# Kernel tuning notes

Hardware: AMD Instinct MI355X
Metric: run time of the kernel (lower is better)

## Reference

```python
import jax, jax.numpy as jnp
import numpy as np

LN_EPS = 1e-5


def _layernorm(x, w, b):
    mu = jnp.mean(x, axis=-1, keepdims=True)
    var = jnp.mean(jnp.square(x - mu), axis=-1, keepdims=True)
    return (x - mu) * jax.lax.rsqrt(var + LN_EPS) * w + b


def setup_inputs() -> dict:
    key = jax.random.key(0)
    ks = jax.random.split(key, 6)
    B, V, P, D = 32, 4, 784, 768
    H = 8
    x = jax.random.normal(ks[0], (B, V * P, D), dtype=jnp.float32)
    s = 0.02  # init scale for weights
    return {
        "x": x,
        "num_views": V,
        "norm1_w": jnp.ones((D,), jnp.float32),
        "norm1_b": jnp.zeros((D,), jnp.float32),
        "in_proj_w": jax.random.normal(ks[1], (3 * D, D), jnp.float32) * s,
        "in_proj_b": jnp.zeros((3 * D,), jnp.float32),
        "out_w": jax.random.normal(ks[2], (D, D), jnp.float32) * s,
        "out_b": jnp.zeros((D,), jnp.float32),
        "norm2_w": jnp.ones((D,), jnp.float32),
        "norm2_b": jnp.zeros((D,), jnp.float32),
        "ffn_w1": jax.random.normal(ks[3], (4 * D, D), jnp.float32) * s,
        "ffn_b1": jnp.zeros((4 * D,), jnp.float32),
        "ffn_w2": jax.random.normal(ks[4], (D, 4 * D), jnp.float32) * s,
        "ffn_b2": jnp.zeros((D,), jnp.float32),
    }


def reference(x, num_views, norm1_w, norm1_b, in_proj_w, in_proj_b, out_w, out_b,
              norm2_w, norm2_b, ffn_w1, ffn_b1, ffn_w2, ffn_b2):
    B, T, D = x.shape
    V = num_views
    P = T // V
    H = 8
    dh = D // H

    # The per-patch python loop in the original is embarrassingly parallel over
    # patches: fold the patch dim into batch -> (B*P, V, D) tokens of seq-len V.
    xv = x.reshape(B, V, P, D).transpose(0, 2, 1, 3).reshape(B * P, V, D)

    # pre-norm cross-view attention (torch MultiheadAttention, batch_first)
    h = _layernorm(xv, norm1_w, norm1_b)
    qkv = h @ in_proj_w.T + in_proj_b                      # (BP, V, 3D)
    q, k, v = jnp.split(qkv, 3, axis=-1)
    q = q.reshape(B * P, V, H, dh).transpose(0, 2, 1, 3)   # (BP, H, V, dh)
    k = k.reshape(B * P, V, H, dh).transpose(0, 2, 1, 3)
    v = v.reshape(B * P, V, H, dh).transpose(0, 2, 1, 3)
    scores = jnp.einsum("bhqd,bhkd->bhqk", q, k) / jnp.sqrt(jnp.float32(dh))
    attn = jax.nn.softmax(scores, axis=-1)
    o = jnp.einsum("bhqk,bhkd->bhqd", attn, v)             # (BP, H, V, dh)
    o = o.transpose(0, 2, 1, 3).reshape(B * P, V, D)
    o = o @ out_w.T + out_b
    xv = xv + o

    # pre-norm FFN with exact (erf) GELU; dropout = identity (eval mode)
    h = _layernorm(xv, norm2_w, norm2_b)
    h = jax.nn.gelu(h @ ffn_w1.T + ffn_b1, approximate=False)
    xv = xv + (h @ ffn_w2.T + ffn_b2)

    # undo the fold: (BP, V, D) -> (B, P, V, D) -> (B, V, P, D) -> (B, T, D)
    return xv.reshape(B, P, V, D).transpose(0, 2, 1, 3).reshape(B, T, D)
```

## Files before the change

### kernel.cpp

```cpp
#include <hip/hip_runtime.h>
#include <hip/hip_bf16.h>
#include <math.h>

typedef __bf16 bf16x8 __attribute__((ext_vector_type(8)));
typedef float  f32x4  __attribute__((ext_vector_type(4)));
typedef unsigned short us8 __attribute__((ext_vector_type(8)));
typedef unsigned short us4 __attribute__((ext_vector_type(4)));
typedef unsigned short ush;

__device__ __forceinline__ unsigned short f2bf(float x) {
  unsigned int u = __float_as_uint(x);
  u += 0x7FFFu + ((u >> 16) & 1u);
  return (unsigned short)(u >> 16);
}
__device__ __forceinline__ float bf2f(unsigned short v) {
  return __uint_as_float(((unsigned int)v) << 16);
}
__device__ __forceinline__ float gelu_t(float x) {
  float y = 0.7978845608028654f * x * (1.0f + 0.044715f * x * x);
  float e = __expf(2.0f * y);
  return x - x / (e + 1.0f);
}


__global__ __launch_bounds__(256) void conv_f32_bf16(const float* __restrict__ s,
                                                     unsigned short* __restrict__ d, int n4) {
  int i = blockIdx.x * 256 + threadIdx.x;
  if (i >= n4) return;
  float4 f = ((const float4*)s)[i];
  ushort4 u;
  u.x = f2bf(f.x); u.y = f2bf(f.y); u.z = f2bf(f.z); u.w = f2bf(f.w);
  ((ushort4*)d)[i] = u;
}

__global__ __launch_bounds__(256) void ln_kernel(const float* __restrict__ src,
                                                 const float* __restrict__ w,
                                                 const float* __restrict__ b,
                                                 unsigned short* __restrict__ dst) {
  const int wv = threadIdx.x >> 6;
  const int lane = threadIdx.x & 63;
  const int n = blockIdx.x * 4 + wv;
  const int bp = n >> 2, v = n & 3;
  const int bb = bp / 784, p = bp - bb * 784;
  const float* row = src + ((size_t)bb * 3136 + (size_t)v * 784 + p) * 768;
  float4 x0 = ((const float4*)row)[lane];
  float4 x1 = ((const float4*)row)[lane + 64];
  float4 x2 = ((const float4*)row)[lane + 128];
  float s  = x0.x + x0.y + x0.z + x0.w + x1.x + x1.y + x1.z + x1.w
           + x2.x + x2.y + x2.z + x2.w;
  float ss = x0.x*x0.x + x0.y*x0.y + x0.z*x0.z + x0.w*x0.w
           + x1.x*x1.x + x1.y*x1.y + x1.z*x1.z + x1.w*x1.w
           + x2.x*x2.x + x2.y*x2.y + x2.z*x2.z + x2.w*x2.w;
  #pragma unroll
  for (int off = 32; off > 0; off >>= 1) {
    s  += __shfl_xor(s,  off, 64);
    ss += __shfl_xor(ss, off, 64);
  }
  const float mu   = s * (1.0f / 768.0f);
  const float rstd = rsqrtf(ss * (1.0f / 768.0f) - mu * mu + 1e-5f);
  unsigned short* drow = dst + (size_t)n * 768;
  #pragma unroll
  for (int seg = 0; seg < 3; ++seg) {
    float4 xs = (seg == 0) ? x0 : (seg == 1) ? x1 : x2;
    float4 w4 = ((const float4*)w)[lane + seg * 64];
    float4 b4 = ((const float4*)b)[lane + seg * 64];
    ushort4 u;
    u.x = f2bf((xs.x - mu) * rstd * w4.x + b4.x);
    u.y = f2bf((xs.y - mu) * rstd * w4.y + b4.y);
    u.z = f2bf((xs.z - mu) * rstd * w4.z + b4.z);
    u.w = f2bf((xs.w - mu) * rstd * w4.w + b4.w);
    ((ushort4*)drow)[lane + seg * 64] = u;
  }
}


#define BARX() do { asm volatile("" ::: "memory"); \
                    __builtin_amdgcn_s_barrier();  \
                    asm volatile("" ::: "memory"); } while (0)
#define WAITVM(N) asm volatile("s_waitcnt vmcnt(" #N ")" ::: "memory")

#define STAGE(ISB, HALF, TT) do {                                             \
  const ush* _g = (ISB) ? gB : gA;                                            \
  const int _l0 = (((TT) & 1) << 15) + ((ISB) ? 16384 : 0) + ((HALF) << 13)   \
                + (w << 9);                                                   \
  const size_t _go = (size_t)(((HALF) << 7) + (w << 3)) * K                   \
                   + ((size_t)(TT) << 6);                                     \
  __builtin_amdgcn_global_load_lds(                                           \
      (const __attribute__((address_space(1))) void*)(_g + _go),              \
      (__attribute__((address_space(3))) void*)(smem + _l0), 16, 0, 0);       \
  __builtin_amdgcn_global_load_lds(                                           \
      (const __attribute__((address_space(1))) void*)(_g + _go + ((size_t)K << 6)), \
      (__attribute__((address_space(3))) void*)(smem + _l0 + 4096), 16, 0, 0);\
} while (0)

#define LDA(HM) do {                                                          \
  _Pragma("unroll")                                                           \
  for (int mi4 = 0; mi4 < 4; ++mi4) {                                         \
    const int m = wm * 64 + (HM) * 128 + mi4 * 16 + l16;                      \
    _Pragma("unroll")                                                         \
    for (int kk = 0; kk < 2; ++kk) {                                          \
      const int q = kk * 4 + quad;                                            \
      af[mi4][kk] = *(const bf16x8*)(smem + aofs + m * 64 + ((q ^ l7) << 3)); \
    }                                                                         \
  }                                                                           \
} while (0)

#define LDB(HN, BF) do {                                                      \
  _Pragma("unroll")                                                           \
  for (int ni2 = 0; ni2 < 2; ++ni2) {                                         \
    const int n = wn * 32 + (HN) * 128 + ni2 * 16 + l16;                      \
    _Pragma("unroll")                                                         \
    for (int kk = 0; kk < 2; ++kk) {                                          \
      const int q = kk * 4 + quad;                                            \
      BF[ni2][kk] = *(const bf16x8*)(smem + bofs + n * 64 + ((q ^ l7) << 3)); \
    }                                                                         \
  }                                                                           \
} while (0)

#define MFMAC(HM, HN, BF) do {                                                \
  __builtin_amdgcn_s_setprio(1);                                              \
  _Pragma("unroll")                                                           \
  for (int mi4 = 0; mi4 < 4; ++mi4)                                           \
    _Pragma("unroll")                                                         \
    for (int ni2 = 0; ni2 < 2; ++ni2)                                         \
      _Pragma("unroll")                                                       \
      for (int kk = 0; kk < 2; ++kk)                                          \
        acc[(HM)*4 + mi4][(HN)*2 + ni2] = __builtin_amdgcn_mfma_f32_16x16x32_bf16( \
            af[mi4][kk], BF[ni2][kk], acc[(HM)*4 + mi4][(HN)*2 + ni2], 0, 0, 0); \
  __builtin_amdgcn_s_setprio(0);                                              \
} while (0)

template <int K, int EPI>
__global__ __launch_bounds__(512, 2) void gemm256(const ush* __restrict__ A,
                                                  const ush* __restrict__ Bm,
                                                  const float* __restrict__ bias,
                                                  void* __restrict__ outp,
                                                  const float* __restrict__ aux,
                                                  int N) {
  __shared__ __attribute__((aligned(16))) ush smem[65536];
  constexpr int NT = K / 64;
  const int tid  = threadIdx.x;
  const int w    = tid >> 6;
  const int lane = tid & 63;
  const int quad = lane >> 4;
  const int l16  = lane & 15;
  const int l7   = l16 & 7;
  const int wm   = w >> 2;
  const int wn   = w & 3;

  const int gx   = gridDim.x;
  const int nwg  = gx * 392;
  const int flat = blockIdx.y * gx + blockIdx.x;
  const int xcd  = flat & 7;
  const int pos  = xcd * (nwg >> 3) + (flat >> 3);
  const int by   = pos / gx;
  const int bx   = pos - by * gx;

  const int r8  = lane >> 3;
  const int cb  = lane & 7;
  const int swo = (cb ^ r8) << 3;
  const ush* gA = A  + (size_t)(by * 256 + r8) * K + swo;
  const ush* gB = Bm + (size_t)(bx * 256 + r8) * K + swo;

  f32x4 acc[8][4];
  #pragma unroll
  for (int i = 0; i < 8; ++i)
    #pragma unroll
    for (int j = 0; j < 4; ++j) {
      f32x4 z = {0.0f, 0.0f, 0.0f, 0.0f};
      acc[i][j] = z;
    }
  bf16x8 af[4][2], bf0[2][2], bf1[2][2];

  STAGE(0, 0, 0); STAGE(1, 0, 0); STAGE(0, 1, 0);
  STAGE(1, 1, 0); STAGE(0, 0, 1); STAGE(1, 0, 1);
  WAITVM(8);
  BARX();

  #pragma unroll 2
  for (int t = 0; t < NT; ++t) {
    const int aofs = (t & 1) << 15;
    const int bofs = aofs + 16384;
    LDA(0); LDB(0, bf0);
    if (t <= NT - 2) STAGE(0, 1, t + 1);
    BARX();
    MFMAC(0, 0, bf0);
    if (t < NT - 1) { WAITVM(6); } else { WAITVM(0); }
    BARX();
    LDB(1, bf1);
    if (t <= NT - 2) STAGE(1, 1, t + 1);
    BARX();
    MFMAC(0, 1, bf1);
    BARX();
    LDA(1);
    if (t <= NT - 3) STAGE(0, 0, t + 2);
    BARX();
    MFMAC(1, 0, bf0);
    BARX();
    if (t <= NT - 3) STAGE(1, 0, t + 2);
    BARX();
    MFMAC(1, 1, bf1);
    if (t <= NT - 3)      { WAITVM(8); }
    else if (t == NT - 2) { WAITVM(4); }
    BARX();
  }

  float* lsm = (float*)smem;
  #pragma unroll
  for (int s = 0; s < 4; ++s) {
    if (wm == (s & 1)) {
      const int hm = s >> 1;
      #pragma unroll
      for (int mi4 = 0; mi4 < 4; ++mi4)
        #pragma unroll
        for (int ni = 0; ni < 4; ++ni) {
          const int col = wn * 32 + (ni >> 1) * 128 + (ni & 1) * 16 + l16;
          #pragma unroll
          for (int r = 0; r < 4; ++r) {
            const int row_l = mi4 * 16 + quad * 4 + r;
            lsm[row_l * 260 + col] = acc[hm * 4 + mi4][ni][r];
          }
        }
    }
    __syncthreads();
    #pragma unroll
    for (int j = 0; j < 8; ++j) {
      const int cc    = tid + 512 * j;
      const int row_l = cc >> 6;
      const int c4    = (cc & 63) << 2;
      f32x4 vv = *(const f32x4*)&lsm[row_l * 260 + c4];
      const int rr    = by * 256 + s * 64 + row_l;
      const int col_g = bx * 256 + c4;
      f32x4 b4 = *(const f32x4*)&bias[col_g];
      vv += b4;
      if (EPI == 0) {
        const int seg = col_g / 768;
        const int c2  = col_g - seg * 768;
        const int hh  = c2 / 96;
        const int dd  = c2 - hh * 96;
        const int bp = rr >> 2, v = rr & 3;
        us4 u = { f2bf(vv[0]), f2bf(vv[1]), f2bf(vv[2]), f2bf(vv[3]) };
        *(us4*)((unsigned short*)outp + (size_t)bp * 9216 + seg * 3072 + hh * 384 + v * 96 + dd) = u;
      } else if (EPI == 1 || EPI == 3) {
        const int bp = rr >> 2, v = rr & 3;
        const int bb = bp / 784, p = bp - bb * 784;
        const size_t addr = ((size_t)bb * 3136 + (size_t)v * 784 + p) * 768 + col_g;
        f32x4 a4 = *(const f32x4*)(aux + addr);
        vv += a4;
        *(f32x4*)((float*)outp + addr) = vv;
      } else {
        us4 u = { f2bf(gelu_t(vv[0])), f2bf(gelu_t(vv[1])),
                  f2bf(gelu_t(vv[2])), f2bf(gelu_t(vv[3])) };
        *(us4*)((unsigned short*)outp + (size_t)rr * N + col_g) = u;
      }
    }
    __syncthreads();
  }
}

__global__ __launch_bounds__(256) void attn_kernel(const unsigned short* __restrict__ qs,
                                                   unsigned short* __restrict__ o) {
  int idx = blockIdx.x * 256 + threadIdx.x;
  int vq = idx & 3;
  int h  = (idx >> 2) & 7;
  int bp = idx >> 5;
  const unsigned short* qp = qs + (size_t)bp * 9216 + h * 384 + vq * 96;
  const unsigned short* kp = qs + (size_t)bp * 9216 + 3072 + h * 384;
  const unsigned short* vp = qs + (size_t)bp * 9216 + 6144 + h * 384;
  float s0 = 0.f, s1 = 0.f, s2 = 0.f, s3 = 0.f;
  #pragma unroll
  for (int c = 0; c < 96; c += 8) {
    us8 q8 = *(const us8*)(qp + c);
    us8 k0 = *(const us8*)(kp + c);
    us8 k1 = *(const us8*)(kp + 96 + c);
    us8 k2 = *(const us8*)(kp + 192 + c);
    us8 k3 = *(const us8*)(kp + 288 + c);
    #pragma unroll
    for (int j = 0; j < 8; ++j) {
      float qf = bf2f(q8[j]);
      s0 += qf * bf2f(k0[j]);
      s1 += qf * bf2f(k1[j]);
      s2 += qf * bf2f(k2[j]);
      s3 += qf * bf2f(k3[j]);
    }
  }
  const float scale = 0.10206207261596575f;
  s0 *= scale; s1 *= scale; s2 *= scale; s3 *= scale;
  float m = fmaxf(fmaxf(s0, s1), fmaxf(s2, s3));
  float e0 = __expf(s0 - m), e1 = __expf(s1 - m), e2 = __expf(s2 - m), e3 = __expf(s3 - m);
  float inv = 1.0f / (e0 + e1 + e2 + e3);
  e0 *= inv; e1 *= inv; e2 *= inv; e3 *= inv;
  unsigned short* op = o + (size_t)(bp * 4 + vq) * 768 + h * 96;
  #pragma unroll
  for (int c = 0; c < 96; c += 8) {
    us8 v0 = *(const us8*)(vp + c);
    us8 v1 = *(const us8*)(vp + 96 + c);
    us8 v2 = *(const us8*)(vp + 192 + c);
    us8 v3 = *(const us8*)(vp + 288 + c);
    us8 r;
    #pragma unroll
    for (int j = 0; j < 8; ++j) {
      float val = e0 * bf2f(v0[j]) + e1 * bf2f(v1[j]) + e2 * bf2f(v2[j]) + e3 * bf2f(v3[j]);
      r[j] = f2bf(val);
    }
    *(us8*)(op + c) = r;
  }
}

extern "C" void kernel_launch(void* const* d_in, const int* in_sizes, int n_in,
                              void* d_out, int out_size, void* d_ws, size_t ws_size,
                              hipStream_t stream) {
  const float* x         = (const float*)d_in[0];
  const float* norm1_w   = (const float*)d_in[2];
  const float* norm1_b   = (const float*)d_in[3];
  const float* in_proj_w = (const float*)d_in[4];
  const float* in_proj_b = (const float*)d_in[5];
  const float* out_w     = (const float*)d_in[6];
  const float* out_b     = (const float*)d_in[7];
  const float* norm2_w   = (const float*)d_in[8];
  const float* norm2_b   = (const float*)d_in[9];
  const float* ffn_w1    = (const float*)d_in[10];
  const float* ffn_b1    = (const float*)d_in[11];
  const float* ffn_w2    = (const float*)d_in[12];
  const float* ffn_b2    = (const float*)d_in[13];
  float* out = (float*)d_out;

  char* ws = (char*)d_ws;
  unsigned short* wq = (unsigned short*)ws;
  unsigned short* wh = (unsigned short*)(ws + 616562688u);
  unsigned short* wB = (unsigned short*)(ws + 616562688u + 154140672u);
  unsigned short* wIn  = wB;
  unsigned short* wOut = wB + 1769472;
  unsigned short* wF1  = wOut + 589824;
  unsigned short* wF2  = wF1 + 2359296;

  conv_f32_bf16<<<(442368 + 255) / 256, 256, 0, stream>>>(in_proj_w, wIn, 442368);
  conv_f32_bf16<<<(147456 + 255) / 256, 256, 0, stream>>>(out_w, wOut, 147456);
  conv_f32_bf16<<<(589824 + 255) / 256, 256, 0, stream>>>(ffn_w1, wF1, 589824);
  conv_f32_bf16<<<(589824 + 255) / 256, 256, 0, stream>>>(ffn_w2, wF2, 589824);

  ln_kernel<<<25088, 256, 0, stream>>>(x, norm1_w, norm1_b, wh);
  gemm256<768, 0><<<dim3(9, 392), 512, 0, stream>>>(wh, wIn, in_proj_b, (void*)wq, nullptr, 2304);
  attn_kernel<<<3136, 256, 0, stream>>>(wq, wh);
  gemm256<768, 1><<<dim3(3, 392), 512, 0, stream>>>(wh, wOut, out_b, (void*)out, x, 768);
  ln_kernel<<<25088, 256, 0, stream>>>(out, norm2_w, norm2_b, wh);
  gemm256<768, 2><<<dim3(12, 392), 512, 0, stream>>>(wh, wF1, ffn_b1, (void*)wq, nullptr, 3072);
  gemm256<3072, 3><<<dim3(3, 392), 512, 0, stream>>>(wq, wF2, ffn_b2, (void*)out, out, 768);

  (void)in_sizes; (void)n_in; (void)out_size; (void)ws_size;
}
```

Baseline: 2.644 ms.

## Make GEMMs persistent with cross-tile prefetch and direct-register epilogue

Replaces the one-block-per-tile GEMM launch with a persistent kernel of 256 blocks. Each block walks a contiguous range of tiles within its XCD and prefetches the next tile's K-slices while finishing the current one, hiding per-tile prologue and tail latency. The epilogue now writes accumulators straight from registers with scalar stores instead of staging them through LDS, which removes barriers but loses vectorized, coalesced stores. The pointer-advance and wait-count logic becomes more complex, and load balance depends on tile counts per XCD.

```diff
diff --git a/kernel.cpp b/kernel.cpp
--- a/kernel.cpp
+++ b/kernel.cpp
@@ -79,17 +79,15 @@
                     asm volatile("" ::: "memory"); } while (0)
 #define WAITVM(N) asm volatile("s_waitcnt vmcnt(" #N ")" ::: "memory")
 
-#define STAGE(ISB, HALF, TT) do {                                             \
-  const ush* _g = (ISB) ? gB : gA;                                            \
-  const int _l0 = (((TT) & 1) << 15) + ((ISB) ? 16384 : 0) + ((HALF) << 13)   \
+#define STAGE2(ISB, HALF, PAR, PTR) do {                                      \
+  const int _l0 = ((PAR) << 15) + ((ISB) ? 16384 : 0) + ((HALF) << 13)        \
                 + (w << 9);                                                   \
-  const size_t _go = (size_t)(((HALF) << 7) + (w << 3)) * K                   \
-                   + ((size_t)(TT) << 6);                                     \
+  const ush* _g = (PTR) + (size_t)(((HALF) << 7) + (w << 3)) * K;             \
   __builtin_amdgcn_global_load_lds(                                           \
-      (const __attribute__((address_space(1))) void*)(_g + _go),              \
+      (const __attribute__((address_space(1))) void*)_g,                      \
       (__attribute__((address_space(3))) void*)(smem + _l0), 16, 0, 0);       \
   __builtin_amdgcn_global_load_lds(                                           \
-      (const __attribute__((address_space(1))) void*)(_g + _go + ((size_t)K << 6)), \
+      (const __attribute__((address_space(1))) void*)(_g + ((size_t)K << 6)), \
       (__attribute__((address_space(3))) void*)(smem + _l0 + 4096), 16, 0, 0);\
 } while (0)
 
@@ -130,13 +128,146 @@
   __builtin_amdgcn_s_setprio(0);                                              \
 } while (0)
 
+#define ZEROACC() do {                                                        \
+  _Pragma("unroll")                                                           \
+  for (int _i = 0; _i < 8; ++_i)                                              \
+    _Pragma("unroll")                                                         \
+    for (int _j = 0; _j < 4; ++_j) { f32x4 _z = {0.f,0.f,0.f,0.f}; acc[_i][_j] = _z; } \
+} while (0)
+
+#define ADV2() do {                                                           \
+  k2 += 64;                                                                   \
+  if (k2 < K) { if (live2) { pA2 += 64; pB2 += 64; } }                        \
+  else {                                                                      \
+    k2 = 0; pos2 += 32;                                                       \
+    if (pos2 < pos_end) {                                                     \
+      const int _by = pos2 / gx, _bx = pos2 - _by * gx;                       \
+      pA2 = A  + (size_t)(_by * 256 + r8) * K + swo;                          \
+      pB2 = Bm + (size_t)(_bx * 256 + r8) * K + swo;                          \
+      live2 = true;                                                           \
+    } else { live2 = false; }                                                 \
+  }                                                                           \
+} while (0)
+
+#define SHIFT() do {                                                          \
+  pA1 = pA2; pB1 = pB2; live1 = live2; k1 = k2; pos1 = pos2;                  \
+  ADV2();                                                                     \
+} while (0)
+
+#define STEP(PAR) do {                                                        \
+  const int aofs = (PAR) << 15;                                               \
+  const int bofs = aofs + 16384;                                              \
+  const bool lastT = (pos_c + 32 >= pos_end);                                 \
+                                                                      \
+  LDA(0); LDB(0, bf0);                                                        \
+  if (live1) { STAGE2(0, 1, (PAR) ^ 1, pA1); }                                \
+  BARX();                                                                     \
+  MFMAC(0, 0, bf0);                                                           \
+  if (lastT && kc == NT - 1) { WAITVM(0); } else { WAITVM(6); }               \
+  BARX();                                                                     \
+                                                                      \
+  LDB(1, bf1);                                                                \
+  if (live1) { STAGE2(1, 1, (PAR) ^ 1, pB1); }                                \
+  BARX();                                                                     \
+  MFMAC(0, 1, bf1);                                                           \
+  BARX();                                                                     \
+                                                                      \
+  LDA(1);                                                                     \
+  if (live2) { STAGE2(0, 0, (PAR), pA2); }                                    \
+  BARX();                                                                     \
+  MFMAC(1, 0, bf0);                                                           \
+  BARX();                                                                     \
+                                                     \
+  if (live2) { STAGE2(1, 0, (PAR), pB2); }                                    \
+  BARX();                                                                     \
+  MFMAC(1, 1, bf1);                                                           \
+  if (!lastT || kc <= NT - 3) { WAITVM(8); }                                  \
+  else if (kc == NT - 2) { WAITVM(4); }                                       \
+  BARX();                                                                     \
+} while (0)
+
+#define EPILOGUE() do {                                                       \
+  const int rb0 = by_c * 256 + wm * 64 + quad * 4;                            \
+  const int cb0 = bx_c * 256 + wn * 32 + l16;                                 \
+  if (EPI == 1 || EPI == 3) {                                                 \
+    size_t rowb[8];                                                           \
+    _Pragma("unroll")                                                         \
+    for (int hm2 = 0; hm2 < 2; ++hm2)                                         \
+      _Pragma("unroll")                                                       \
+      for (int mi4 = 0; mi4 < 4; ++mi4) {                                     \
+        const int bp = (rb0 + hm2 * 128 + mi4 * 16) >> 2;                     \
+        const int bb = bp / 784, p = bp - bb * 784;                           \
+        rowb[hm2 * 4 + mi4] = ((size_t)bb * 3136 + p) * 768;                  \
+      }                                                                       \
+    _Pragma("unroll")                                                         \
+    for (int hn = 0; hn < 2; ++hn)                                            \
+      _Pragma("unroll")                                                       \
+      for (int ni2 = 0; ni2 < 2; ++ni2) {                                     \
+        const int col = cb0 + hn * 128 + ni2 * 16;                            \
+        const float bv = bias[col];                                           \
+        _Pragma("unroll")                                                     \
+        for (int hm2 = 0; hm2 < 2; ++hm2)                                     \
+          _Pragma("unroll")                                                   \
+          for (int mi4 = 0; mi4 < 4; ++mi4) {                                 \
+            const size_t ba = rowb[hm2 * 4 + mi4] + col;                      \
+            _Pragma("unroll")                                                 \
+            for (int r = 0; r < 4; ++r) {                                     \
+              const size_t ad = ba + (size_t)r * 602112;                      \
+              ((float*)outp)[ad] = acc[hm2*4+mi4][hn*2+ni2][r] + bv + aux[ad];\
+            }                                                                 \
+          }                                                                   \
+      }                                                                       \
+  } else if (EPI == 0) {                                                      \
+    _Pragma("unroll")                                                         \
+    for (int hn = 0; hn < 2; ++hn)                                            \
+      _Pragma("unroll")                                                       \
+      for (int ni2 = 0; ni2 < 2; ++ni2) {                                     \
+        const int col = cb0 + hn * 128 + ni2 * 16;                            \
+        const int seg = col / 768;                                            \
+        const int c2  = col - seg * 768;                                      \
+        const int hh  = c2 / 96;                                              \
+        const int dd  = c2 - hh * 96;                                         \
+        const int colb = seg * 3072 + hh * 384 + dd;                          \
+        const float bv = bias[col];                                           \
+        _Pragma("unroll")                                                     \
+        for (int hm2 = 0; hm2 < 2; ++hm2)                                     \
+          _Pragma("unroll")                                                   \
+          for (int mi4 = 0; mi4 < 4; ++mi4) {                                 \
+            const int bp = (rb0 + hm2 * 128 + mi4 * 16) >> 2;                 \
+            unsigned short* ob = (unsigned short*)outp + (size_t)bp * 9216 + colb; \
+            _Pragma("unroll")                                                 \
+            for (int r = 0; r < 4; ++r)                                       \
+              ob[r * 96] = f2bf(acc[hm2*4+mi4][hn*2+ni2][r] + bv);            \
+          }                                                                   \
+      }                                                                       \
+  } else {                              \
+    _Pragma("unroll")                                                         \
+    for (int hn = 0; hn < 2; ++hn)                                            \
+      _Pragma("unroll")                                                       \
+      for (int ni2 = 0; ni2 < 2; ++ni2) {                                     \
+        const int col = cb0 + hn * 128 + ni2 * 16;                            \
+        const float bv = bias[col];                                           \
+        _Pragma("unroll")                                                     \
+        for (int hm2 = 0; hm2 < 2; ++hm2)                                     \
+          _Pragma("unroll")                                                   \
+          for (int mi4 = 0; mi4 < 4; ++mi4) {                                 \
+            const int rr = rb0 + hm2 * 128 + mi4 * 16;                        \
+            unsigned short* ob = (unsigned short*)outp + (size_t)rr * N + col;\
+            _Pragma("unroll")                                                 \
+            for (int r = 0; r < 4; ++r)                                       \
+              ob[(size_t)r * N] = f2bf(gelu_t(acc[hm2*4+mi4][hn*2+ni2][r] + bv)); \
+          }                                                                   \
+      }                                                                       \
+  }                                                                           \
+} while (0)
+
 template <int K, int EPI>
-__global__ __launch_bounds__(512, 2) void gemm256(const ush* __restrict__ A,
-                                                  const ush* __restrict__ Bm,
-                                                  const float* __restrict__ bias,
-                                                  void* __restrict__ outp,
-                                                  const float* __restrict__ aux,
-                                                  int N) {
+__global__ __launch_bounds__(512, 2) void gemm_p(const ush* __restrict__ A,
+                                                 const ush* __restrict__ Bm,
+                                                 const float* __restrict__ bias,
+                                                 void* __restrict__ outp,
+                                                 const float* __restrict__ aux,
+                                                 int N, int gx, int nwg) {
   __shared__ __attribute__((aligned(16))) ush smem[65536];
   constexpr int NT = K / 64;
   const int tid  = threadIdx.x;
@@ -148,113 +279,58 @@
   const int wm   = w >> 2;
   const int wn   = w & 3;
 
-  const int gx   = gridDim.x;
-  const int nwg  = gx * 392;
-  const int flat = blockIdx.y * gx + blockIdx.x;
-  const int xcd  = flat & 7;
-  const int pos  = xcd * (nwg >> 3) + (flat >> 3);
-  const int by   = pos / gx;
-  const int bx   = pos - by * gx;
+  const int bid = blockIdx.x;
+  const int xcd = bid & 7;
+  const int cu  = bid >> 3;
+  const int tpx = nwg >> 3;
+  int pos_c = xcd * tpx + cu;
+  const int pos_end = (xcd + 1) * tpx;
+  if (pos_c >= pos_end) return;
+
+  int by_c = pos_c / gx, bx_c = pos_c - by_c * gx;
 
   const int r8  = lane >> 3;
   const int cb  = lane & 7;
   const int swo = (cb ^ r8) << 3;
-  const ush* gA = A  + (size_t)(by * 256 + r8) * K + swo;
-  const ush* gB = Bm + (size_t)(bx * 256 + r8) * K + swo;
+
+  const ush* pA0 = A  + (size_t)(by_c * 256 + r8) * K + swo;
+  const ush* pB0 = Bm + (size_t)(bx_c * 256 + r8) * K + swo;
+  int pos1 = pos_c, k1 = 0;
+  const ush* pA1 = pA0; const ush* pB1 = pB0; bool live1 = true;
+  {
+    k1 = 64; pA1 += 64; pB1 += 64;
+  }
+  int pos2 = pos1, k2 = k1;
+  const ush* pA2 = pA1; const ush* pB2 = pB1; bool live2 = true;
+  ADV2();
 
   f32x4 acc[8][4];
-  #pragma unroll
-  for (int i = 0; i < 8; ++i)
-    #pragma unroll
-    for (int j = 0; j < 4; ++j) {
-      f32x4 z = {0.0f, 0.0f, 0.0f, 0.0f};
-      acc[i][j] = z;
-    }
+  ZEROACC();
   bf16x8 af[4][2], bf0[2][2], bf1[2][2];
 
-  STAGE(0, 0, 0); STAGE(1, 0, 0); STAGE(0, 1, 0);
-  STAGE(1, 1, 0); STAGE(0, 0, 1); STAGE(1, 0, 1);
+  STAGE2(0, 0, 0, pA0); STAGE2(1, 0, 0, pB0);
+  STAGE2(0, 1, 0, pA0); STAGE2(1, 1, 0, pB0);
+  STAGE2(0, 0, 1, pA1); STAGE2(1, 0, 1, pB1);
   WAITVM(8);
   BARX();
 
-  #pragma unroll 2
-  for (int t = 0; t < NT; ++t) {
-    const int aofs = (t & 1) << 15;
-    const int bofs = aofs + 16384;
-    LDA(0); LDB(0, bf0);
-    if (t <= NT - 2) STAGE(0, 1, t + 1);
-    BARX();
-    MFMAC(0, 0, bf0);
-    if (t < NT - 1) { WAITVM(6); } else { WAITVM(0); }
-    BARX();
-    LDB(1, bf1);
-    if (t <= NT - 2) STAGE(1, 1, t + 1);
-    BARX();
-    MFMAC(0, 1, bf1);
-    BARX();
-    LDA(1);
-    if (t <= NT - 3) STAGE(0, 0, t + 2);
-    BARX();
-    MFMAC(1, 0, bf0);
-    BARX();
-    if (t <= NT - 3) STAGE(1, 0, t + 2);
-    BARX();
-    MFMAC(1, 1, bf1);
-    if (t <= NT - 3)      { WAITVM(8); }
-    else if (t == NT - 2) { WAITVM(4); }
-    BARX();
-  }
-
-  float* lsm = (float*)smem;
-  #pragma unroll
-  for (int s = 0; s < 4; ++s) {
-    if (wm == (s & 1)) {
-      const int hm = s >> 1;
-      #pragma unroll
-      for (int mi4 = 0; mi4 < 4; ++mi4)
-        #pragma unroll
-        for (int ni = 0; ni < 4; ++ni) {
-          const int col = wn * 32 + (ni >> 1) * 128 + (ni & 1) * 16 + l16;
-          #pragma unroll
-          for (int r = 0; r < 4; ++r) {
-            const int row_l = mi4 * 16 + quad * 4 + r;
-            lsm[row_l * 260 + col] = acc[hm * 4 + mi4][ni][r];
-          }
-        }
+  int kc = 0;
+  for (;;) {
+    STEP(0);
+    ++kc;
+    SHIFT();
+    STEP(1);
+    if (kc == NT - 1) {
+      EPILOGUE();
+      pos_c += 32;
+      if (pos_c >= pos_end) break;
+      kc = 0;
+      by_c = pos_c / gx; bx_c = pos_c - by_c * gx;
+      ZEROACC();
+    } else {
+      ++kc;
     }
-    __syncthreads();
-    #pragma unroll
-    for (int j = 0; j < 8; ++j) {
-      const int cc    = tid + 512 * j;
-      const int row_l = cc >> 6;
-      const int c4    = (cc & 63) << 2;
-      f32x4 vv = *(const f32x4*)&lsm[row_l * 260 + c4];
-      const int rr    = by * 256 + s * 64 + row_l;
-      const int col_g = bx * 256 + c4;
-      f32x4 b4 = *(const f32x4*)&bias[col_g];
-      vv += b4;
-      if (EPI == 0) {
-        const int seg = col_g / 768;
-        const int c2  = col_g - seg * 768;
-        const int hh  = c2 / 96;
-        const int dd  = c2 - hh * 96;
-        const int bp = rr >> 2, v = rr & 3;
-        us4 u = { f2bf(vv[0]), f2bf(vv[1]), f2bf(vv[2]), f2bf(vv[3]) };
-        *(us4*)((unsigned short*)outp + (size_t)bp * 9216 + seg * 3072 + hh * 384 + v * 96 + dd) = u;
-      } else if (EPI == 1 || EPI == 3) {
-        const int bp = rr >> 2, v = rr & 3;
-        const int bb = bp / 784, p = bp - bb * 784;
-        const size_t addr = ((size_t)bb * 3136 + (size_t)v * 784 + p) * 768 + col_g;
-        f32x4 a4 = *(const f32x4*)(aux + addr);
-        vv += a4;
-        *(f32x4*)((float*)outp + addr) = vv;
-      } else {
-        us4 u = { f2bf(gelu_t(vv[0])), f2bf(gelu_t(vv[1])),
-                  f2bf(gelu_t(vv[2])), f2bf(gelu_t(vv[3])) };
-        *(us4*)((unsigned short*)outp + (size_t)rr * N + col_g) = u;
-      }
-    }
-    __syncthreads();
+    SHIFT();
   }
 }
 
@@ -340,12 +416,12 @@
   conv_f32_bf16<<<(589824 + 255) / 256, 256, 0, stream>>>(ffn_w2, wF2, 589824);
 
   ln_kernel<<<25088, 256, 0, stream>>>(x, norm1_w, norm1_b, wh);
-  gemm256<768, 0><<<dim3(9, 392), 512, 0, stream>>>(wh, wIn, in_proj_b, (void*)wq, nullptr, 2304);
+  gemm_p<768, 0><<<256, 512, 0, stream>>>(wh, wIn, in_proj_b, (void*)wq, nullptr, 2304, 9, 3528);
   attn_kernel<<<3136, 256, 0, stream>>>(wq, wh);
-  gemm256<768, 1><<<dim3(3, 392), 512, 0, stream>>>(wh, wOut, out_b, (void*)out, x, 768);
+  gemm_p<768, 1><<<256, 512, 0, stream>>>(wh, wOut, out_b, (void*)out, x, 768, 3, 1176);
   ln_kernel<<<25088, 256, 0, stream>>>(out, norm2_w, norm2_b, wh);
-  gemm256<768, 2><<<dim3(12, 392), 512, 0, stream>>>(wh, wF1, ffn_b1, (void*)wq, nullptr, 3072);
-  gemm256<3072, 3><<<dim3(3, 392), 512, 0, stream>>>(wq, wF2, ffn_b2, (void*)out, out, 768);
+  gemm_p<768, 2><<<256, 512, 0, stream>>>(wh, wF1, ffn_b1, (void*)wq, nullptr, 3072, 12, 4704);
+  gemm_p<3072, 3><<<256, 512, 0, stream>>>(wq, wF2, ffn_b2, (void*)out, out, 768, 3, 1176);
 
   (void)in_sizes; (void)n_in; (void)out_size; (void)ws_size;
 }
```

New measurement: 2.978 ms. +12.6%, slower.

## Store GEMM A operands in pre-tiled swizzled layout for contiguous LDS staging

Applied to the files above, without the earlier changes.

The producers of GEMM A operands (layernorm, attention output, GELU epilogue) now write bf16 activations in a blocked layout of 256-row by 64-column tiles with the XOR swizzle already applied. The GEMM's A staging then loads each tile as one contiguous 32KB chunk per k-step instead of strided row reads, and the LDS read swizzle is keyed on the row index. This is meant to improve global-load coalescing and reduce address arithmetic for the A loads. In exchange, the producer writes become scattered, and the layout assumes the row count is a multiple of 256.

```diff
diff --git a/kernel.cpp b/kernel.cpp
--- a/kernel.cpp
+++ b/kernel.cpp
@@ -58,18 +58,20 @@
   }
   const float mu   = s * (1.0f / 768.0f);
   const float rstd = rsqrtf(ss * (1.0f / 768.0f) - mu * mu + 1e-5f);
-  unsigned short* drow = dst + (size_t)n * 768;
+  const int r = n & 255;
+  unsigned short* bb2 = dst + (((size_t)(n >> 8) * 12) << 14) + r * 64
+                      + ((((lane >> 1) & 7) ^ (r & 7)) << 3) + ((lane & 1) << 2);
   #pragma unroll
   for (int seg = 0; seg < 3; ++seg) {
     float4 xs = (seg == 0) ? x0 : (seg == 1) ? x1 : x2;
     float4 w4 = ((const float4*)w)[lane + seg * 64];
     float4 b4 = ((const float4*)b)[lane + seg * 64];
-    ushort4 u;
-    u.x = f2bf((xs.x - mu) * rstd * w4.x + b4.x);
-    u.y = f2bf((xs.y - mu) * rstd * w4.y + b4.y);
-    u.z = f2bf((xs.z - mu) * rstd * w4.z + b4.z);
-    u.w = f2bf((xs.w - mu) * rstd * w4.w + b4.w);
-    ((ushort4*)drow)[lane + seg * 64] = u;
+    us4 u;
+    u[0] = f2bf((xs.x - mu) * rstd * w4.x + b4.x);
+    u[1] = f2bf((xs.y - mu) * rstd * w4.y + b4.y);
+    u[2] = f2bf((xs.z - mu) * rstd * w4.z + b4.z);
+    u[3] = f2bf((xs.w - mu) * rstd * w4.w + b4.w);
+    *(us4*)(bb2 + (((size_t)((lane >> 4) + seg * 4)) << 14)) = u;
   }
 }
 
@@ -79,17 +81,27 @@
                     asm volatile("" ::: "memory"); } while (0)
 #define WAITVM(N) asm volatile("s_waitcnt vmcnt(" #N ")" ::: "memory")
 
-#define STAGE(ISB, HALF, TT) do {                                             \
-  const ush* _g = (ISB) ? gB : gA;                                            \
-  const int _l0 = (((TT) & 1) << 15) + ((ISB) ? 16384 : 0) + ((HALF) << 13)   \
-                + (w << 9);                                                   \
-  const size_t _go = (size_t)(((HALF) << 7) + (w << 3)) * K                   \
-                   + ((size_t)(TT) << 6);                                     \
+#define STAGE_A(HALF, TT) do {                                                \
+  _Pragma("unroll")                                                           \
+  for (int _j = 0; _j < 2; ++_j) {                                            \
+    const int _ob = ((HALF) << 13) + (w << 10) + (_j << 9);                   \
+    __builtin_amdgcn_global_load_lds(                                         \
+        (const __attribute__((address_space(1))) void*)(                      \
+            gAt + (((size_t)(TT)) << 14) + _ob + lnoff8),                     \
+        (__attribute__((address_space(3))) void*)(                            \
+            smem + ((((TT) & 1)) << 15) + _ob), 16, 0, 0);                    \
+  }                                                                           \
+} while (0)
+
+#define STAGE_B(HALF, TT) do {                                                \
+  const int _l0 = ((((TT) & 1)) << 15) + 16384 + ((HALF) << 13) + (w << 9);   \
+  const ush* _g = gB + (size_t)(((HALF) << 7) + (w << 3)) * K                 \
+                + (((size_t)(TT)) << 6);                                      \
   __builtin_amdgcn_global_load_lds(                                           \
-      (const __attribute__((address_space(1))) void*)(_g + _go),              \
+      (const __attribute__((address_space(1))) void*)_g,                      \
       (__attribute__((address_space(3))) void*)(smem + _l0), 16, 0, 0);       \
   __builtin_amdgcn_global_load_lds(                                           \
-      (const __attribute__((address_space(1))) void*)(_g + _go + ((size_t)K << 6)), \
+      (const __attribute__((address_space(1))) void*)(_g + ((size_t)K << 6)), \
       (__attribute__((address_space(3))) void*)(smem + _l0 + 4096), 16, 0, 0);\
 } while (0)
 
@@ -100,7 +112,7 @@
     _Pragma("unroll")                                                         \
     for (int kk = 0; kk < 2; ++kk) {                                          \
       const int q = kk * 4 + quad;                                            \
-      af[mi4][kk] = *(const bf16x8*)(smem + aofs + m * 64 + ((q ^ l7) << 3)); \
+      af[mi4][kk] = *(const bf16x8*)(smem + aofs + m * 64 + ((q ^ (m & 7)) << 3)); \
     }                                                                         \
   }                                                                           \
 } while (0)
@@ -112,7 +124,7 @@
     _Pragma("unroll")                                                         \
     for (int kk = 0; kk < 2; ++kk) {                                          \
       const int q = kk * 4 + quad;                                            \
-      BF[ni2][kk] = *(const bf16x8*)(smem + bofs + n * 64 + ((q ^ l7) << 3)); \
+      BF[ni2][kk] = *(const bf16x8*)(smem + bofs + n * 64 + ((q ^ (n & 7)) << 3)); \
     }                                                                         \
   }                                                                           \
 } while (0)
@@ -144,7 +156,6 @@
   const int lane = tid & 63;
   const int quad = lane >> 4;
   const int l16  = lane & 15;
-  const int l7   = l16 & 7;
   const int wm   = w >> 2;
   const int wn   = w & 3;
 
@@ -156,10 +167,12 @@
   const int by   = pos / gx;
   const int bx   = pos - by * gx;
 
+  const ush* gAt   = A + (((size_t)by * NT) << 14);
+  const int  lnoff8 = lane << 3;
+
   const int r8  = lane >> 3;
   const int cb  = lane & 7;
   const int swo = (cb ^ r8) << 3;
-  const ush* gA = A  + (size_t)(by * 256 + r8) * K + swo;
   const ush* gB = Bm + (size_t)(bx * 256 + r8) * K + swo;
 
   f32x4 acc[8][4];
@@ -172,8 +185,8 @@
     }
   bf16x8 af[4][2], bf0[2][2], bf1[2][2];
 
-  STAGE(0, 0, 0); STAGE(1, 0, 0); STAGE(0, 1, 0);
-  STAGE(1, 1, 0); STAGE(0, 0, 1); STAGE(1, 0, 1);
+  STAGE_A(0, 0); STAGE_B(0, 0); STAGE_A(1, 0);
+  STAGE_B(1, 0); STAGE_A(0, 1); STAGE_B(0, 1);
   WAITVM(8);
   BARX();
 
@@ -182,22 +195,22 @@
     const int aofs = (t & 1) << 15;
     const int bofs = aofs + 16384;
     LDA(0); LDB(0, bf0);
-    if (t <= NT - 2) STAGE(0, 1, t + 1);
+    if (t <= NT - 2) STAGE_A(1, t + 1);
     BARX();
     MFMAC(0, 0, bf0);
     if (t < NT - 1) { WAITVM(6); } else { WAITVM(0); }
     BARX();
     LDB(1, bf1);
-    if (t <= NT - 2) STAGE(1, 1, t + 1);
+    if (t <= NT - 2) STAGE_B(1, t + 1);
     BARX();
     MFMAC(0, 1, bf1);
     BARX();
     LDA(1);
-    if (t <= NT - 3) STAGE(0, 0, t + 2);
+    if (t <= NT - 3) STAGE_A(0, t + 2);
     BARX();
     MFMAC(1, 0, bf0);
     BARX();
-    if (t <= NT - 3) STAGE(1, 0, t + 2);
+    if (t <= NT - 3) STAGE_B(0, t + 2);
     BARX();
     MFMAC(1, 1, bf1);
     if (t <= NT - 3)      { WAITVM(8); }
@@ -251,7 +264,10 @@
       } else {
         us4 u = { f2bf(gelu_t(vv[0])), f2bf(gelu_t(vv[1])),
                   f2bf(gelu_t(vv[2])), f2bf(gelu_t(vv[3])) };
-        *(us4*)((unsigned short*)outp + (size_t)rr * N + col_g) = u;
+        const int rb = rr & 255;
+        *(us4*)((unsigned short*)outp
+               + (((size_t)(rr >> 8) * 48 + (col_g >> 6)) << 14)
+               + rb * 64 + ((((col_g >> 3) & 7) ^ (rb & 7)) << 3) + (col_g & 7)) = u;
       }
     }
     __syncthreads();
@@ -290,7 +306,9 @@
   float e0 = __expf(s0 - m), e1 = __expf(s1 - m), e2 = __expf(s2 - m), e3 = __expf(s3 - m);
   float inv = 1.0f / (e0 + e1 + e2 + e3);
   e0 *= inv; e1 *= inv; e2 *= inv; e3 *= inv;
-  unsigned short* op = o + (size_t)(bp * 4 + vq) * 768 + h * 96;
+  const int rn = bp * 4 + vq;
+  const int rr2 = rn & 255;
+  unsigned short* ob = o + (((size_t)(rn >> 8) * 12) << 14) + rr2 * 64;
   #pragma unroll
   for (int c = 0; c < 96; c += 8) {
     us8 v0 = *(const us8*)(vp + c);
@@ -303,7 +321,8 @@
       float val = e0 * bf2f(v0[j]) + e1 * bf2f(v1[j]) + e2 * bf2f(v2[j]) + e3 * bf2f(v3[j]);
       r[j] = f2bf(val);
     }
-    *(us8*)(op + c) = r;
+    const int k = h * 96 + c;
+    *(us8*)(ob + (((size_t)(k >> 6)) << 14) + ((((k >> 3) & 7) ^ (rr2 & 7)) << 3)) = r;
   }
 }
 
```

After: 2.691 ms. Within noise of the previous version (+1.8%).
